# Kernel tuning notes

Measured on AMD Instinct MI355X. Metric: run time of the kernel, lower is better.

The kernel has to match this reference:

```python
import jax, jax.numpy as jnp
import numpy as np

ALPHA = 0.3  # LeakyReLU slope


def setup_inputs() -> dict:
    key = jax.random.key(0)
    k1, k2, k3, k4 = jax.random.split(key, 4)
    B, S, F, H = 256, 8, 2048, 8
    inputs = jax.random.normal(k1, (B, S, F), dtype=jnp.float32)
    # GlorotNormal-ish scale for W: std = sqrt(2/(2F+F))
    W = jax.random.normal(k2, (H, 2 * F, F), dtype=jnp.float32) * np.float32(np.sqrt(2.0 / (3 * F)))
    att_w = jax.random.normal(k3, (H, F), dtype=jnp.float32) * np.float32(np.sqrt(2.0 / (F + 1)))
    bias = jax.random.normal(k4, (H, F), dtype=jnp.float32) * 0.01
    return {"inputs": inputs, "W": W, "att_w": att_w, "bias": bias}


def reference(inputs, W, att_w, bias):
    # inputs: [B,S,F]; W: [H,2F,F]; att_w: [H,F]; bias: [H,F]
    B, S, F = inputs.shape
    # h_chunk = node 0 features repeated along seq axis, concat with h -> [B,S,2F]
    h_chunk = jnp.broadcast_to(inputs[:, :1, :], (B, S, F))
    h_cat = jnp.concatenate([h_chunk, inputs], axis=-1)
    # per-head projection + LeakyReLU (GATv2 ordering): [B,H,S,F]
    Wh = jax.nn.leaky_relu(jnp.einsum('bsc,hcf->bhsf', h_cat, W), negative_slope=ALPHA)
    # attention scores e: [B,H,S]; softmax over seq axis (axis=1 in original layout)
    e = jnp.einsum('bhsf,hf->bhs', Wh, att_w)
    attn = jax.nn.softmax(e, axis=-1)
    # broadcast-multiply, bias add, residual, identity activation
    att_out = attn[..., None] * Wh + bias[None, :, None, :] + inputs[:, None, :, :]
    # sum over heads / num_heads == mean over heads
    return att_out.mean(axis=1)
```

## Files before the change

### kernel.cpp

```cpp
#include <hip/hip_runtime.h>
#include <stdint.h>


typedef __attribute__((ext_vector_type(4))) float f32x4;
typedef __attribute__((ext_vector_type(8))) short bf16x8;
typedef __attribute__((ext_vector_type(4))) unsigned short u16x4;
typedef unsigned short u16;
typedef unsigned int u32;

#define LRELU_ALPHA 0.3f

__device__ __forceinline__ u16 bf16_rn(float x) {
  u32 u = __float_as_uint(x);
  u32 r = 0x7FFFu + ((u >> 16) & 1u);
  return (u16)((u + r) >> 16);
}
__device__ __forceinline__ float bf16_to_f32(u16 h) {
  return __uint_as_float(((u32)h) << 16);
}

__global__ __launch_bounds__(256) void split_x_kernel(
    const float* __restrict__ X, u16* __restrict__ Xhi, u16* __restrict__ Xlo) {
  int idx = (blockIdx.x * 256 + threadIdx.x) * 4;
  f32x4 v = *(const f32x4*)&X[idx];
  u16x4 hi, lo;
#pragma unroll
  for (int j = 0; j < 4; ++j) {
    u16 h = bf16_rn(v[j]);
    hi[j] = h;
    lo[j] = bf16_rn(v[j] - bf16_to_f32(h));
  }
  *(u16x4*)&Xhi[idx] = hi;
  *(u16x4*)&Xlo[idx] = lo;
}

__global__ __launch_bounds__(256) void transpose_split_w(
    const float* __restrict__ W, u16* __restrict__ Whi, u16* __restrict__ Wlo) {
  __shared__ float tile[64][65];
  int bid = blockIdx.x;
  int h = bid >> 11;
  int t = bid & 2047;
  int ct = t & 63;
  int ft = t >> 6;
  int c0 = ct << 6, f0 = ft << 6;
  int tid = threadIdx.x;
  int rr = tid >> 4;
  int q4 = (tid & 15) << 2;
  const float* src = W + (size_t)(h * 4096 + c0) * 2048 + f0;
#pragma unroll
  for (int it = 0; it < 4; ++it) {
    int r = it * 16 + rr;
    f32x4 v = *(const f32x4*)&src[(size_t)r * 2048 + q4];
    tile[r][q4] = v[0]; tile[r][q4 + 1] = v[1];
    tile[r][q4 + 2] = v[2]; tile[r][q4 + 3] = v[3];
  }
  __syncthreads();
  size_t dst = (size_t)(h * 2048 + f0) * 4096 + c0;
#pragma unroll
  for (int it = 0; it < 4; ++it) {
    int fr = it * 16 + rr;
    u16x4 hi, lo;
#pragma unroll
    for (int j = 0; j < 4; ++j) {
      float a = tile[q4 + j][fr];
      u16 hb = bf16_rn(a);
      hi[j] = hb;
      lo[j] = bf16_rn(a - bf16_to_f32(hb));
    }
    *(u16x4*)&Whi[dst + (size_t)fr * 4096 + q4] = hi;
    *(u16x4*)&Wlo[dst + (size_t)fr * 4096 + q4] = lo;
  }
}

__device__ __forceinline__ void gl_lds16(const u16* g, u16* l) {
  __builtin_amdgcn_global_load_lds(
      (const __attribute__((address_space(1))) void*)g,
      (__attribute__((address_space(3))) void*)l, 16, 0, 0);
}

#define BAR()    asm volatile("s_barrier" ::: "memory")
#define VM4BAR() asm volatile("s_waitcnt vmcnt(4)\n\ts_barrier" ::: "memory")
#define VM0BAR() asm volatile("s_waitcnt vmcnt(0)\n\ts_barrier" ::: "memory")

template <int AST, bool EPI2>
__global__ __launch_bounds__(512, 2) void gemm3p(
    const u16* __restrict__ Ahi, const u16* __restrict__ Alo,
    const u16* __restrict__ Bhi, const u16* __restrict__ Blo,
    const float* __restrict__ proj0, float* __restrict__ C,
    int Mdim, int koff) {
  __shared__ alignas(16) u16 lAh[2][8192];
  __shared__ alignas(16) u16 lAl[2][8192];
  __shared__ alignas(16) u16 lBh[2][8192];
  __shared__ alignas(16) u16 lBl[2][8192];

  const int tid = threadIdx.x;
  const int lane = tid & 63;
  const int w = tid >> 6;

  const int nwg = gridDim.x;
  const int bid = blockIdx.x;
  const int wg = (bid & 7) * (nwg >> 3) + (bid >> 3);
  const int MT = Mdim >> 8;
  const int nt = wg / MT;
  const int mt = wg - nt * MT;
  const int m0 = mt << 8, n0 = nt << 8;

  const int c0i = 2 * w, c1i = 2 * w + 1;
  const int r0 = c0i * 16 + (lane >> 2);
  const int r1 = c1i * 16 + (lane >> 2);
  const int ul0 = ((lane & 3) - (r0 >> 1)) & 3;
  const int ul1 = ((lane & 3) - (r1 >> 1)) & 3;
  const size_t sA0 = (size_t)(m0 + r0) * AST + ul0 * 8;
  const size_t sA1 = (size_t)(m0 + r1) * AST + ul1 * 8;
  const size_t sB0 = (size_t)(n0 + r0) * 4096 + (size_t)koff + ul0 * 8;
  const size_t sB1 = (size_t)(n0 + r1) * 4096 + (size_t)koff + ul1 * 8;
  const int cw0 = c0i * 512, cw1 = c1i * 512;

  auto stageHi = [&](int b, size_t ko) {
    gl_lds16(Ahi + sA0 + ko, &lAh[b][cw0]);
    gl_lds16(Ahi + sA1 + ko, &lAh[b][cw1]);
    gl_lds16(Bhi + sB0 + ko, &lBh[b][cw0]);
    gl_lds16(Bhi + sB1 + ko, &lBh[b][cw1]);
  };
  auto stageLo = [&](int b, size_t ko) {
    gl_lds16(Alo + sA0 + ko, &lAl[b][cw0]);
    gl_lds16(Alo + sA1 + ko, &lAl[b][cw1]);
    gl_lds16(Blo + sB0 + ko, &lBl[b][cw0]);
    gl_lds16(Blo + sB1 + ko, &lBl[b][cw1]);
  };

  const int frow = lane & 15, kgrp = lane >> 4;
  const int wr = w >> 2, wc = w & 3;
  int aoff[8], boff[4];
#pragma unroll
  for (int i = 0; i < 8; ++i) {
    int r = wr * 128 + i * 16 + frow;
    aoff[i] = r * 32 + ((kgrp + (r >> 1)) & 3) * 8;
  }
#pragma unroll
  for (int j = 0; j < 4; ++j) {
    int r = wc * 64 + j * 16 + frow;
    boff[j] = r * 32 + ((kgrp + (r >> 1)) & 3) * 8;
  }

  f32x4 acc[8][4];
#pragma unroll
  for (int i = 0; i < 8; ++i)
#pragma unroll
    for (int j = 0; j < 4; ++j) acc[i][j] = (f32x4){0.f, 0.f, 0.f, 0.f};

  stageHi(0, 0);
  stageLo(0, 0);
  VM4BAR();

  bf16x8 ah[8], al[8], bh[4], bl[4];

  for (int kt = 0; kt < 63; ++kt) {
    const int p = kt & 1, q = p ^ 1;
    const size_t ko = (size_t)(kt + 1) * 32;
#pragma unroll
    for (int i = 0; i < 8; ++i) ah[i] = *(const bf16x8*)&lAh[p][aoff[i]];
#pragma unroll
    for (int j = 0; j < 4; ++j) bh[j] = *(const bf16x8*)&lBh[p][boff[j]];
    stageHi(q, ko);
    BAR();
    __builtin_amdgcn_s_setprio(1);
#pragma unroll
    for (int i = 0; i < 8; ++i)
#pragma unroll
      for (int j = 0; j < 4; ++j)
        acc[i][j] = __builtin_amdgcn_mfma_f32_16x16x32_bf16(ah[i], bh[j], acc[i][j], 0, 0, 0);
    __builtin_amdgcn_s_setprio(0);
    VM4BAR();

#pragma unroll
    for (int j = 0; j < 4; ++j) bl[j] = *(const bf16x8*)&lBl[p][boff[j]];
    stageLo(q, ko);
    BAR();
    __builtin_amdgcn_s_setprio(1);
#pragma unroll
    for (int i = 0; i < 8; ++i)
#pragma unroll
      for (int j = 0; j < 4; ++j)
        acc[i][j] = __builtin_amdgcn_mfma_f32_16x16x32_bf16(ah[i], bl[j], acc[i][j], 0, 0, 0);
    __builtin_amdgcn_s_setprio(0);
    BAR();

#pragma unroll
    for (int i = 0; i < 8; ++i) al[i] = *(const bf16x8*)&lAl[p][aoff[i]];
    BAR();
    __builtin_amdgcn_s_setprio(1);
#pragma unroll
    for (int i = 0; i < 8; ++i)
#pragma unroll
      for (int j = 0; j < 4; ++j)
        acc[i][j] = __builtin_amdgcn_mfma_f32_16x16x32_bf16(al[i], bh[j], acc[i][j], 0, 0, 0);
    __builtin_amdgcn_s_setprio(0);
    VM4BAR();
  }

  VM0BAR();
  {
    const int p = 1;
#pragma unroll
    for (int i = 0; i < 8; ++i) ah[i] = *(const bf16x8*)&lAh[p][aoff[i]];
#pragma unroll
    for (int j = 0; j < 4; ++j) bh[j] = *(const bf16x8*)&lBh[p][boff[j]];
#pragma unroll
    for (int j = 0; j < 4; ++j) bl[j] = *(const bf16x8*)&lBl[p][boff[j]];
#pragma unroll
    for (int i = 0; i < 8; ++i) al[i] = *(const bf16x8*)&lAl[p][aoff[i]];
#pragma unroll
    for (int i = 0; i < 8; ++i)
#pragma unroll
      for (int j = 0; j < 4; ++j) {
        acc[i][j] = __builtin_amdgcn_mfma_f32_16x16x32_bf16(ah[i], bh[j], acc[i][j], 0, 0, 0);
        acc[i][j] = __builtin_amdgcn_mfma_f32_16x16x32_bf16(ah[i], bl[j], acc[i][j], 0, 0, 0);
        acc[i][j] = __builtin_amdgcn_mfma_f32_16x16x32_bf16(al[i], bh[j], acc[i][j], 0, 0, 0);
      }
  }

#pragma unroll
  for (int i = 0; i < 8; ++i) {
    const int gmb = m0 + wr * 128 + i * 16 + kgrp * 4;
#pragma unroll
    for (int j = 0; j < 4; ++j) {
      const int gn = n0 + wc * 64 + j * 16 + frow;
#pragma unroll
      for (int r = 0; r < 4; ++r) {
        float v = acc[i][j][r];
        const int gm = gmb + r;
        if constexpr (EPI2) {
          v += proj0[(size_t)(gm >> 3) * 16384 + gn];
          v = v > 0.f ? v : v * LRELU_ALPHA;
        }
        C[(size_t)gm * 16384 + gn] = v;
      }
    }
  }
}

__global__ __launch_bounds__(256) void esoftmax_kernel(
    const float* __restrict__ Wh, const float* __restrict__ att_w,
    float* __restrict__ attn) {
  int bid = blockIdx.x;
  int b = bid >> 3, h = bid & 7;
  int tid = threadIdx.x, lane = tid & 63, w = tid >> 6;
  __shared__ float ev[8];
  const float* aw = att_w + h * 2048;
#pragma unroll
  for (int si = 0; si < 2; ++si) {
    int s = w * 2 + si;
    const float* row = Wh + (size_t)((b * 8 + s) * 8 + h) * 2048;
    float sum = 0.f;
#pragma unroll
    for (int i = 0; i < 8; ++i) {
      int idx = (i * 64 + lane) * 4;
      f32x4 rv = *(const f32x4*)&row[idx];
      f32x4 av = *(const f32x4*)&aw[idx];
      sum += rv[0] * av[0] + rv[1] * av[1] + rv[2] * av[2] + rv[3] * av[3];
    }
#pragma unroll
    for (int off = 32; off > 0; off >>= 1) sum += __shfl_down(sum, off, 64);
    if (lane == 0) ev[s] = sum;
  }
  __syncthreads();
  if (tid == 0) {
    float mx = ev[0];
#pragma unroll
    for (int s = 1; s < 8; ++s) mx = fmaxf(mx, ev[s]);
    float ex[8], den = 0.f;
#pragma unroll
    for (int s = 0; s < 8; ++s) { ex[s] = expf(ev[s] - mx); den += ex[s]; }
    float inv = 1.f / den;
#pragma unroll
    for (int s = 0; s < 8; ++s) attn[b * 64 + h * 8 + s] = ex[s] * inv;
  }
}

__global__ __launch_bounds__(256) void out_kernel(
    const float* __restrict__ X, const float* __restrict__ bias,
    const float* __restrict__ Wh, const float* __restrict__ attn,
    float* __restrict__ out) {
  int bid = blockIdx.x;
  int m = bid >> 1;
  int half = bid & 1;
  int b = m >> 3, s = m & 7;
  int f0 = half * 1024 + threadIdx.x * 4;
  __shared__ float a_sm[8];
  if (threadIdx.x < 8) a_sm[threadIdx.x] = attn[b * 64 + threadIdx.x * 8 + s];
  __syncthreads();
  f32x4 acc = *(const f32x4*)&X[(size_t)m * 2048 + f0];
  f32x4 hs = {0.f, 0.f, 0.f, 0.f};
#pragma unroll
  for (int h = 0; h < 8; ++h) {
    f32x4 wv = *(const f32x4*)&Wh[(size_t)m * 16384 + h * 2048 + f0];
    f32x4 bv = *(const f32x4*)&bias[h * 2048 + f0];
    hs += wv * a_sm[h] + bv;
  }
  acc += hs * 0.125f;
  *(f32x4*)&out[(size_t)m * 2048 + f0] = acc;
}

extern "C" void kernel_launch(void* const* d_in, const int* in_sizes, int n_in,
                              void* d_out, int out_size, void* d_ws, size_t ws_size,
                              hipStream_t stream) {
  const float* X = (const float*)d_in[0];
  const float* W = (const float*)d_in[1];
  const float* att_w = (const float*)d_in[2];
  const float* bias = (const float*)d_in[3];
  float* out = (float*)d_out;

  char* ws = (char*)d_ws;
  u16* Whi = (u16*)ws;
  u16* Wlo = (u16*)(ws + 134217728ull);
  u16* Xhi = (u16*)(ws + 268435456ull);
  u16* Xlo = (u16*)(ws + 276824064ull);
  float* proj0 = (float*)(ws + 285212672ull);
  float* Wh = (float*)(ws + 301989888ull);
  float* attn = (float*)(ws + 436207616ull);

  split_x_kernel<<<4096, 256, 0, stream>>>(X, Xhi, Xlo);
  transpose_split_w<<<16384, 256, 0, stream>>>(W, Whi, Wlo);
  gemm3p<16384, false><<<64, 512, 0, stream>>>(Xhi, Xlo, Whi, Wlo, nullptr, proj0, 256, 0);
  gemm3p<2048, true><<<512, 512, 0, stream>>>(Xhi, Xlo, Whi, Wlo, proj0, Wh, 2048, 2048);
  esoftmax_kernel<<<2048, 256, 0, stream>>>(Wh, att_w, attn);
  out_kernel<<<4096, 256, 0, stream>>>(X, bias, Wh, attn, out);
}
```

Measured before the change: 966.1 us.

## Fuse attention scores into GEMM epilogue, retile transpose and small GEMM

Computes the attention-score dot product inside the second GEMM's epilogue with shuffle reductions and atomics into a zeroed score buffer. This removes the separate esoftmax kernel and its re-read of the large Wh tensor, and the softmax moves into out_kernel. The transpose kernel now uses 128x64 tiles with vectorised LDS reads. The first GEMM gets a smaller M tile so it launches more workgroups, and the lo-part loads are merged into one phase with fewer barriers. The atomics make the score sums order-nondeterministic, and the memset adds a launch.

```diff
diff --git a/kernel.cpp b/kernel.cpp
--- a/kernel.cpp
+++ b/kernel.cpp
@@ -10,13 +10,18 @@
 
 #define LRELU_ALPHA 0.3f
 
+struct HL { u16 h, l; };
 __device__ __forceinline__ u16 bf16_rn(float x) {
   u32 u = __float_as_uint(x);
   u32 r = 0x7FFFu + ((u >> 16) & 1u);
   return (u16)((u + r) >> 16);
 }
-__device__ __forceinline__ float bf16_to_f32(u16 h) {
-  return __uint_as_float(((u32)h) << 16);
+__device__ __forceinline__ HL split_rn(float x) {
+  HL r;
+  r.h = bf16_rn(x);
+  float hv = __uint_as_float(((u32)r.h) << 16);
+  r.l = bf16_rn(x - hv);
+  return r;
 }
 
 __global__ __launch_bounds__(256) void split_x_kernel(
@@ -26,9 +31,9 @@
   u16x4 hi, lo;
 #pragma unroll
   for (int j = 0; j < 4; ++j) {
-    u16 h = bf16_rn(v[j]);
-    hi[j] = h;
-    lo[j] = bf16_rn(v[j] - bf16_to_f32(h));
+    HL r = split_rn(v[j]);
+    hi[j] = r.h;
+    lo[j] = r.l;
   }
   *(u16x4*)&Xhi[idx] = hi;
   *(u16x4*)&Xlo[idx] = lo;
@@ -36,39 +41,45 @@
 
 __global__ __launch_bounds__(256) void transpose_split_w(
     const float* __restrict__ W, u16* __restrict__ Whi, u16* __restrict__ Wlo) {
-  __shared__ float tile[64][65];
-  int bid = blockIdx.x;
-  int h = bid >> 11;
-  int t = bid & 2047;
-  int ct = t & 63;
-  int ft = t >> 6;
-  int c0 = ct << 6, f0 = ft << 6;
-  int tid = threadIdx.x;
-  int rr = tid >> 4;
-  int q4 = (tid & 15) << 2;
-  const float* src = W + (size_t)(h * 4096 + c0) * 2048 + f0;
-#pragma unroll
-  for (int it = 0; it < 4; ++it) {
-    int r = it * 16 + rr;
-    f32x4 v = *(const f32x4*)&src[(size_t)r * 2048 + q4];
-    tile[r][q4] = v[0]; tile[r][q4 + 1] = v[1];
-    tile[r][q4 + 2] = v[2]; tile[r][q4 + 3] = v[3];
+  __shared__ float tile[64][132];
+  const int bid = blockIdx.x;
+  const int ct = bid & 31;
+  const int ft = (bid >> 5) & 31;
+  const int h = bid >> 10;
+  const int c0 = ct << 7, f0 = ft << 6;
+  const int tid = threadIdx.x;
+
+  {
+    const int fo = (tid & 15) * 4;
+    const int crb = tid >> 4;
+    const float* src = W + ((size_t)(h * 4096 + c0) * 2048) + f0 + fo;
+#pragma unroll
+    for (int it = 0; it < 8; ++it) {
+      const int cr = it * 16 + crb;
+      f32x4 v = *(const f32x4*)&src[(size_t)cr * 2048];
+#pragma unroll
+      for (int j = 0; j < 4; ++j) tile[fo + j][cr] = v[j];
+    }
   }
   __syncthreads();
-  size_t dst = (size_t)(h * 2048 + f0) * 4096 + c0;
-#pragma unroll
-  for (int it = 0; it < 4; ++it) {
-    int fr = it * 16 + rr;
-    u16x4 hi, lo;
-#pragma unroll
-    for (int j = 0; j < 4; ++j) {
-      float a = tile[q4 + j][fr];
-      u16 hb = bf16_rn(a);
-      hi[j] = hb;
-      lo[j] = bf16_rn(a - bf16_to_f32(hb));
+  {
+    const int c4 = (tid & 31) * 4;
+    const int flb = tid >> 5;
+    const size_t dbase = (size_t)(h * 2048 + f0) * 4096 + c0 + c4;
+#pragma unroll
+    for (int it = 0; it < 8; ++it) {
+      const int fl = it * 8 + flb;
+      f32x4 v = *(const f32x4*)&tile[fl][c4];
+      u16x4 hi, lo;
+#pragma unroll
+      for (int j = 0; j < 4; ++j) {
+        HL r = split_rn(v[j]);
+        hi[j] = r.h;
+        lo[j] = r.l;
+      }
+      *(u16x4*)&Whi[dbase + (size_t)fl * 4096] = hi;
+      *(u16x4*)&Wlo[dbase + (size_t)fl * 4096] = lo;
     }
-    *(u16x4*)&Whi[dst + (size_t)fr * 4096 + q4] = hi;
-    *(u16x4*)&Wlo[dst + (size_t)fr * 4096 + q4] = lo;
   }
 }
 
@@ -78,18 +89,28 @@
       (__attribute__((address_space(3))) void*)l, 16, 0, 0);
 }
 
-#define BAR()    asm volatile("s_barrier" ::: "memory")
-#define VM4BAR() asm volatile("s_waitcnt vmcnt(4)\n\ts_barrier" ::: "memory")
-#define VM0BAR() asm volatile("s_waitcnt vmcnt(0)\n\ts_barrier" ::: "memory")
-
-template <int AST, bool EPI2>
-__global__ __launch_bounds__(512, 2) void gemm3p(
+template <int N> __device__ __forceinline__ void vm_bar();
+template <> __device__ __forceinline__ void vm_bar<4>() {
+  asm volatile("s_waitcnt vmcnt(4)\n\ts_barrier" ::: "memory");
+}
+template <> __device__ __forceinline__ void vm_bar<3>() {
+  asm volatile("s_waitcnt vmcnt(3)\n\ts_barrier" ::: "memory");
+}
+template <> __device__ __forceinline__ void vm_bar<0>() {
+  asm volatile("s_waitcnt vmcnt(0)\n\ts_barrier" ::: "memory");
+}
+#define BAR() asm volatile("s_barrier" ::: "memory")
+
+template <int AST, bool EPI2, int WM>
+__global__ __launch_bounds__(512, 2) void gemm2p(
     const u16* __restrict__ Ahi, const u16* __restrict__ Alo,
     const u16* __restrict__ Bhi, const u16* __restrict__ Blo,
     const float* __restrict__ proj0, float* __restrict__ C,
+    const float* __restrict__ att_w, float* __restrict__ e,
     int Mdim, int koff) {
-  __shared__ alignas(16) u16 lAh[2][8192];
-  __shared__ alignas(16) u16 lAl[2][8192];
+  constexpr int VMN = WM / 4 + 2;
+  __shared__ alignas(16) u16 lAh[2][WM * 1024];
+  __shared__ alignas(16) u16 lAl[2][WM * 1024];
   __shared__ alignas(16) u16 lBh[2][8192];
   __shared__ alignas(16) u16 lBl[2][8192];
 
@@ -100,41 +121,47 @@
   const int nwg = gridDim.x;
   const int bid = blockIdx.x;
   const int wg = (bid & 7) * (nwg >> 3) + (bid >> 3);
-  const int MT = Mdim >> 8;
+  const int MT = Mdim / (WM * 32);
   const int nt = wg / MT;
   const int mt = wg - nt * MT;
-  const int m0 = mt << 8, n0 = nt << 8;
-
-  const int c0i = 2 * w, c1i = 2 * w + 1;
-  const int r0 = c0i * 16 + (lane >> 2);
-  const int r1 = c1i * 16 + (lane >> 2);
-  const int ul0 = ((lane & 3) - (r0 >> 1)) & 3;
-  const int ul1 = ((lane & 3) - (r1 >> 1)) & 3;
-  const size_t sA0 = (size_t)(m0 + r0) * AST + ul0 * 8;
-  const size_t sA1 = (size_t)(m0 + r1) * AST + ul1 * 8;
-  const size_t sB0 = (size_t)(n0 + r0) * 4096 + (size_t)koff + ul0 * 8;
-  const size_t sB1 = (size_t)(n0 + r1) * 4096 + (size_t)koff + ul1 * 8;
-  const int cw0 = c0i * 512, cw1 = c1i * 512;
+  const int m0 = mt * (WM * 32), n0 = nt << 8;
+
+  const int rB0 = w * 32 + (lane >> 2);
+  const int rB1 = rB0 + 16;
+  const int ulB0 = ((lane & 3) - (rB0 >> 1)) & 3;
+  const int ulB1 = ((lane & 3) - (rB1 >> 1)) & 3;
+  const size_t sB0 = (size_t)(n0 + rB0) * 4096 + (size_t)koff + ulB0 * 8;
+  const size_t sB1 = (size_t)(n0 + rB1) * 4096 + (size_t)koff + ulB1 * 8;
+  const int cwB0 = w * 1024, cwB1 = cwB0 + 512;
+
+  const int rA0 = (WM == 8) ? (w * 32 + (lane >> 2)) : (w * 16 + (lane >> 2));
+  const int rA1 = rA0 + 16;
+  const int ulA0 = ((lane & 3) - (rA0 >> 1)) & 3;
+  const int ulA1 = ((lane & 3) - (rA1 >> 1)) & 3;
+  const size_t sA0 = (size_t)(m0 + rA0) * AST + ulA0 * 8;
+  const size_t sA1 = (size_t)(m0 + rA1) * AST + ulA1 * 8;
+  const int cwA0 = (WM == 8) ? (w * 1024) : (w * 512);
+  const int cwA1 = cwA0 + 512;
 
   auto stageHi = [&](int b, size_t ko) {
-    gl_lds16(Ahi + sA0 + ko, &lAh[b][cw0]);
-    gl_lds16(Ahi + sA1 + ko, &lAh[b][cw1]);
-    gl_lds16(Bhi + sB0 + ko, &lBh[b][cw0]);
-    gl_lds16(Bhi + sB1 + ko, &lBh[b][cw1]);
+    gl_lds16(Ahi + sA0 + ko, &lAh[b][cwA0]);
+    if constexpr (WM == 8) gl_lds16(Ahi + sA1 + ko, &lAh[b][cwA1]);
+    gl_lds16(Bhi + sB0 + ko, &lBh[b][cwB0]);
+    gl_lds16(Bhi + sB1 + ko, &lBh[b][cwB1]);
   };
   auto stageLo = [&](int b, size_t ko) {
-    gl_lds16(Alo + sA0 + ko, &lAl[b][cw0]);
-    gl_lds16(Alo + sA1 + ko, &lAl[b][cw1]);
-    gl_lds16(Blo + sB0 + ko, &lBl[b][cw0]);
-    gl_lds16(Blo + sB1 + ko, &lBl[b][cw1]);
+    gl_lds16(Alo + sA0 + ko, &lAl[b][cwA0]);
+    if constexpr (WM == 8) gl_lds16(Alo + sA1 + ko, &lAl[b][cwA1]);
+    gl_lds16(Blo + sB0 + ko, &lBl[b][cwB0]);
+    gl_lds16(Blo + sB1 + ko, &lBl[b][cwB1]);
   };
 
   const int frow = lane & 15, kgrp = lane >> 4;
   const int wr = w >> 2, wc = w & 3;
-  int aoff[8], boff[4];
-#pragma unroll
-  for (int i = 0; i < 8; ++i) {
-    int r = wr * 128 + i * 16 + frow;
+  int aoff[WM], boff[4];
+#pragma unroll
+  for (int i = 0; i < WM; ++i) {
+    int r = wr * (WM * 16) + i * 16 + frow;
     aoff[i] = r * 32 + ((kgrp + (r >> 1)) & 3) * 8;
   }
 #pragma unroll
@@ -143,75 +170,70 @@
     boff[j] = r * 32 + ((kgrp + (r >> 1)) & 3) * 8;
   }
 
-  f32x4 acc[8][4];
-#pragma unroll
-  for (int i = 0; i < 8; ++i)
+  f32x4 acc[WM][4];
+#pragma unroll
+  for (int i = 0; i < WM; ++i)
 #pragma unroll
     for (int j = 0; j < 4; ++j) acc[i][j] = (f32x4){0.f, 0.f, 0.f, 0.f};
 
   stageHi(0, 0);
   stageLo(0, 0);
-  VM4BAR();
-
-  bf16x8 ah[8], al[8], bh[4], bl[4];
+  vm_bar<VMN>();
+
+  bf16x8 ah[WM], al[WM], bh[4], bl[4];
 
   for (int kt = 0; kt < 63; ++kt) {
     const int p = kt & 1, q = p ^ 1;
     const size_t ko = (size_t)(kt + 1) * 32;
 #pragma unroll
-    for (int i = 0; i < 8; ++i) ah[i] = *(const bf16x8*)&lAh[p][aoff[i]];
+    for (int i = 0; i < WM; ++i) ah[i] = *(const bf16x8*)&lAh[p][aoff[i]];
 #pragma unroll
     for (int j = 0; j < 4; ++j) bh[j] = *(const bf16x8*)&lBh[p][boff[j]];
     stageHi(q, ko);
     BAR();
     __builtin_amdgcn_s_setprio(1);
 #pragma unroll
-    for (int i = 0; i < 8; ++i)
+    for (int i = 0; i < WM; ++i)
 #pragma unroll
       for (int j = 0; j < 4; ++j)
         acc[i][j] = __builtin_amdgcn_mfma_f32_16x16x32_bf16(ah[i], bh[j], acc[i][j], 0, 0, 0);
     __builtin_amdgcn_s_setprio(0);
-    VM4BAR();
+    vm_bar<VMN>();
 
 #pragma unroll
     for (int j = 0; j < 4; ++j) bl[j] = *(const bf16x8*)&lBl[p][boff[j]];
+#pragma unroll
+    for (int i = 0; i < WM; ++i) al[i] = *(const bf16x8*)&lAl[p][aoff[i]];
     stageLo(q, ko);
     BAR();
     __builtin_amdgcn_s_setprio(1);
 #pragma unroll
-    for (int i = 0; i < 8; ++i)
+    for (int i = 0; i < WM; ++i)
 #pragma unroll
       for (int j = 0; j < 4; ++j)
         acc[i][j] = __builtin_amdgcn_mfma_f32_16x16x32_bf16(ah[i], bl[j], acc[i][j], 0, 0, 0);
-    __builtin_amdgcn_s_setprio(0);
-    BAR();
-
-#pragma unroll
-    for (int i = 0; i < 8; ++i) al[i] = *(const bf16x8*)&lAl[p][aoff[i]];
-    BAR();
-    __builtin_amdgcn_s_setprio(1);
-#pragma unroll
-    for (int i = 0; i < 8; ++i)
+#pragma unroll
+    for (int i = 0; i < WM; ++i)
 #pragma unroll
       for (int j = 0; j < 4; ++j)
         acc[i][j] = __builtin_amdgcn_mfma_f32_16x16x32_bf16(al[i], bh[j], acc[i][j], 0, 0, 0);
     __builtin_amdgcn_s_setprio(0);
-    VM4BAR();
-  }
-
-  VM0BAR();
+    vm_bar<VMN>();
+  }
+
+  vm_bar<0>();
   {
     const int p = 1;
 #pragma unroll
-    for (int i = 0; i < 8; ++i) ah[i] = *(const bf16x8*)&lAh[p][aoff[i]];
+    for (int i = 0; i < WM; ++i) ah[i] = *(const bf16x8*)&lAh[p][aoff[i]];
 #pragma unroll
     for (int j = 0; j < 4; ++j) bh[j] = *(const bf16x8*)&lBh[p][boff[j]];
 #pragma unroll
     for (int j = 0; j < 4; ++j) bl[j] = *(const bf16x8*)&lBl[p][boff[j]];
 #pragma unroll
-    for (int i = 0; i < 8; ++i) al[i] = *(const bf16x8*)&lAl[p][aoff[i]];
-#pragma unroll
-    for (int i = 0; i < 8; ++i)
+    for (int i = 0; i < WM; ++i) al[i] = *(const bf16x8*)&lAl[p][aoff[i]];
+#pragma unroll
+    for (int i = 0; i < WM; ++i)
 #pragma unroll
       for (int j = 0; j < 4; ++j) {
         acc[i][j] = __builtin_amdgcn_mfma_f32_16x16x32_bf16(ah[i], bh[j], acc[i][j], 0, 0, 0);
@@ -220,76 +242,73 @@
       }
   }
 
-#pragma unroll
-  for (int i = 0; i < 8; ++i) {
-    const int gmb = m0 + wr * 128 + i * 16 + kgrp * 4;
+  float aw0, aw1, aw2, aw3;
+  if constexpr (EPI2) {
+    aw0 = att_w[n0 + wc * 64 + 0 * 16 + frow];
+    aw1 = att_w[n0 + wc * 64 + 1 * 16 + frow];
+    aw2 = att_w[n0 + wc * 64 + 2 * 16 + frow];
+    aw3 = att_w[n0 + wc * 64 + 3 * 16 + frow];
+  }
+#pragma unroll
+  for (int i = 0; i < WM; ++i) {
+    const int gmb = m0 + wr * (WM * 16) + i * 16 + kgrp * 4;
+    float vv[4][4];
 #pragma unroll
     for (int j = 0; j < 4; ++j) {
       const int gn = n0 + wc * 64 + j * 16 + frow;
 #pragma unroll
       for (int r = 0; r < 4; ++r) {
         float v = acc[i][j][r];
-        const int gm = gmb + r;
         if constexpr (EPI2) {
-          v += proj0[(size_t)(gm >> 3) * 16384 + gn];
+          v += proj0[(size_t)((gmb + r) >> 3) * 16384 + gn];
           v = v > 0.f ? v : v * LRELU_ALPHA;
         }
-        C[(size_t)gm * 16384 + gn] = v;
+        vv[j][r] = v;
+        C[(size_t)(gmb + r) * 16384 + gn] = v;
       }
     }
-  }
-}
-
-__global__ __launch_bounds__(256) void esoftmax_kernel(
-    const float* __restrict__ Wh, const float* __restrict__ att_w,
-    float* __restrict__ attn) {
-  int bid = blockIdx.x;
-  int b = bid >> 3, h = bid & 7;
-  int tid = threadIdx.x, lane = tid & 63, w = tid >> 6;
-  __shared__ float ev[8];
-  const float* aw = att_w + h * 2048;
-#pragma unroll
-  for (int si = 0; si < 2; ++si) {
-    int s = w * 2 + si;
-    const float* row = Wh + (size_t)((b * 8 + s) * 8 + h) * 2048;
-    float sum = 0.f;
-#pragma unroll
-    for (int i = 0; i < 8; ++i) {
-      int idx = (i * 64 + lane) * 4;
-      f32x4 rv = *(const f32x4*)&row[idx];
-      f32x4 av = *(const f32x4*)&aw[idx];
-      sum += rv[0] * av[0] + rv[1] * av[1] + rv[2] * av[2] + rv[3] * av[3];
+    if constexpr (EPI2) {
+#pragma unroll
+      for (int r = 0; r < 4; ++r) {
+        float psum = vv[0][r] * aw0 + vv[1][r] * aw1 + vv[2][r] * aw2 + vv[3][r] * aw3;
+        psum += __shfl_xor(psum, 1, 16);
+        psum += __shfl_xor(psum, 2, 16);
+        psum += __shfl_xor(psum, 4, 16);
+        psum += __shfl_xor(psum, 8, 16);
+        if ((lane & 15) == 0) {
+          const int gm = gmb + r;
+          atomicAdd(&e[(gm >> 3) * 64 + (n0 >> 11) * 8 + (gm & 7)], psum);
+        }
+      }
     }
-#pragma unroll
-    for (int off = 32; off > 0; off >>= 1) sum += __shfl_down(sum, off, 64);
-    if (lane == 0) ev[s] = sum;
-  }
-  __syncthreads();
-  if (tid == 0) {
-    float mx = ev[0];
-#pragma unroll
-    for (int s = 1; s < 8; ++s) mx = fmaxf(mx, ev[s]);
-    float ex[8], den = 0.f;
-#pragma unroll
-    for (int s = 0; s < 8; ++s) { ex[s] = expf(ev[s] - mx); den += ex[s]; }
-    float inv = 1.f / den;
-#pragma unroll
-    for (int s = 0; s < 8; ++s) attn[b * 64 + h * 8 + s] = ex[s] * inv;
   }
 }
 
 __global__ __launch_bounds__(256) void out_kernel(
     const float* __restrict__ X, const float* __restrict__ bias,
-    const float* __restrict__ Wh, const float* __restrict__ attn,
+    const float* __restrict__ Wh, const float* __restrict__ e,
     float* __restrict__ out) {
   int bid = blockIdx.x;
   int m = bid >> 1;
   int half = bid & 1;
   int b = m >> 3, s = m & 7;
-  int f0 = half * 1024 + threadIdx.x * 4;
+  int tid = threadIdx.x;
   __shared__ float a_sm[8];
-  if (threadIdx.x < 8) a_sm[threadIdx.x] = attn[b * 64 + threadIdx.x * 8 + s];
+  if (tid < 8) {
+    const float* eb = e + b * 64 + tid * 8;
+    float ev[8];
+#pragma unroll
+    for (int k = 0; k < 8; ++k) ev[k] = eb[k];
+    float mx = ev[0];
+#pragma unroll
+    for (int k = 1; k < 8; ++k) mx = fmaxf(mx, ev[k]);
+    float den = 0.f;
+#pragma unroll
+    for (int k = 0; k < 8; ++k) den += expf(ev[k] - mx);
+    a_sm[tid] = expf(ev[s] - mx) / den;
+  }
   __syncthreads();
+  int f0 = half * 1024 + tid * 4;
   f32x4 acc = *(const f32x4*)&X[(size_t)m * 2048 + f0];
   f32x4 hs = {0.f, 0.f, 0.f, 0.f};
 #pragma unroll
@@ -318,12 +337,14 @@
   u16* Xlo = (u16*)(ws + 276824064ull);
   float* proj0 = (float*)(ws + 285212672ull);
   float* Wh = (float*)(ws + 301989888ull);
-  float* attn = (float*)(ws + 436207616ull);
+  float* e = (float*)(ws + 436207616ull);
 
   split_x_kernel<<<4096, 256, 0, stream>>>(X, Xhi, Xlo);
-  transpose_split_w<<<16384, 256, 0, stream>>>(W, Whi, Wlo);
-  gemm3p<16384, false><<<64, 512, 0, stream>>>(Xhi, Xlo, Whi, Wlo, nullptr, proj0, 256, 0);
-  gemm3p<2048, true><<<512, 512, 0, stream>>>(Xhi, Xlo, Whi, Wlo, proj0, Wh, 2048, 2048);
-  esoftmax_kernel<<<2048, 256, 0, stream>>>(Wh, att_w, attn);
-  out_kernel<<<4096, 256, 0, stream>>>(X, bias, Wh, attn, out);
-}
+  transpose_split_w<<<8192, 256, 0, stream>>>(W, Whi, Wlo);
+  (void)hipMemsetAsync(e, 0, 65536, stream);
+  gemm2p<16384, false, 4><<<128, 512, 0, stream>>>(
+      Xhi, Xlo, Whi, Wlo, nullptr, proj0, nullptr, nullptr, 256, 0);
+  gemm2p<2048, true, 8><<<512, 512, 0, stream>>>(
+      Xhi, Xlo, Whi, Wlo, proj0, Wh, att_w, e, 2048, 2048);
+  out_kernel<<<4096, 256, 0, stream>>>(X, bias, Wh, e, out);
+}
```

After: 873.5 us. 9.6% less time.
